# Kernel optimization log

Hardware: AMD Instinct MI355X
Metric: run time of the kernel (lower is better)

## Reference

```python
import jax, jax.numpy as jnp
import numpy as np

B, N, NODE_DIM, COND_DIM, EDGE_DIM = 32, 96, 2048, 1024, 128


def _wn_linear(x, v, g, b):
    # weight-normed linear: W = g * v / ||v||_row  (torch nn.utils.weight_norm, dim=0)
    w = v * (g / jnp.linalg.norm(v, axis=1))[:, None]
    return x @ w.T + b


def setup_inputs() -> dict:
    key = jax.random.key(0)
    ks = jax.random.split(key, 6)

    def lin(k, out_d, in_d):
        k1, k2, k3 = jax.random.split(k, 3)
        v = jax.random.normal(k1, (out_d, in_d), jnp.float32) * (1.0 / np.sqrt(in_d))
        g = jax.random.uniform(k2, (out_d,), jnp.float32, 0.5, 1.5)
        b = jax.random.normal(k3, (out_d,), jnp.float32) * 0.01
        return v, g, b

    node_feats = jax.random.normal(ks[0], (B, N, NODE_DIM), jnp.float32)
    cond_feats = jax.random.normal(ks[1], (B, COND_DIM), jnp.float32)

    # edge indexes: flat indices into the [B*N*N] pairwise tensor, self-loops removed
    i, j = np.meshgrid(np.arange(N), np.arange(N), indexing='ij')
    pair = (i * N + j)[i != j]                                  # [N*(N-1)]
    edge_indexes = (np.arange(B)[:, None] * N * N + pair[None, :]).reshape(-1)
    edge_indexes = jnp.asarray(edge_indexes, dtype=jnp.int32)   # [B*N*(N-1)]

    node_v, node_g, node_b = lin(ks[2], EDGE_DIM, NODE_DIM)
    joint_v, joint_g, joint_b = lin(ks[3], EDGE_DIM, 2 * EDGE_DIM)
    q_v, q_g, q_b = lin(ks[4], EDGE_DIM, COND_DIM)
    lin_v, lin_g, lin_b = lin(ks[5], EDGE_DIM, 2 * EDGE_DIM)

    return {
        'node_feats': node_feats, 'cond_feats': cond_feats, 'edge_indexes': edge_indexes,
        'node_v': node_v, 'node_g': node_g, 'node_b': node_b,
        'joint_v': joint_v, 'joint_g': joint_g, 'joint_b': joint_b,
        'q_v': q_v, 'q_g': q_g, 'q_b': q_b,
        'lin_v': lin_v, 'lin_g': lin_g, 'lin_b': lin_b,
    }


def reference(node_feats, cond_feats, edge_indexes,
              node_v, node_g, node_b,
              joint_v, joint_g, joint_b,
              q_v, q_g, q_b,
              lin_v, lin_g, lin_b):
    b_n, n_n, _ = node_feats.shape
    # node projection (dropout p=0 -> identity)
    h = jax.nn.relu(_wn_linear(node_feats, node_v, node_g, node_b))   # [B, N, E]

    # node_intersect('cat') builds [B,N,N,2E] then flattens; we gather the
    # selected edges directly by decomposing the flat indices (same math).
    nn2 = n_n * n_n
    bi = edge_indexes // nn2
    rem = edge_indexes % nn2
    ii = rem // n_n
    jj = rem % n_n
    fusion = jnp.concatenate([h[bi, ii], h[bi, jj]], axis=-1)         # [Edges, 2E]

    joint = jax.nn.relu(_wn_linear(fusion, joint_v, joint_g, joint_b))  # [Edges, E]
    q = jax.nn.relu(_wn_linear(cond_feats, q_v, q_g, q_b))              # [B, E]

    e_per = joint.shape[0] // b_n
    o_c = joint.shape[1]
    jb = joint.reshape(b_n, e_per, o_c)
    qb = jnp.broadcast_to(q[:, None, :], (b_n, e_per, o_c))
    cat = jnp.concatenate([jb, qb], axis=-1)                           # [B, Eper, 2E]
    out = jax.nn.relu(_wn_linear(cat, lin_v, lin_g, lin_b))            # [B, Eper, E]
    return out.reshape(b_n * e_per, o_c)
```

## Files before the change

### kernel.cpp

```cpp
#include <hip/hip_runtime.h>
#include <hip/hip_bf16.h>


#define WS_BIAS      256
#define WS_WN_NODE   4096
#define WS_WN_JOINT  528384
#define WS_WN_Q      593920
#define WS_WN_LIN    856064
#define WS_H         921600
#define WS_P         1708032
#define WS_Q         3280896
#define WS_QC        4853760

typedef __bf16 bf16x8 __attribute__((ext_vector_type(8)));
typedef float  f32x4  __attribute__((ext_vector_type(4)));

union BF8 { bf16x8 v; ushort u[8]; uint4 q; };

__device__ __forceinline__ float b2f(ushort u){ union{uint i; float f;} c; c.i=(uint)u<<16; return c.f; }
__device__ __forceinline__ ushort f2b(float f){ union{float f; uint i;} c; c.f=f; uint i=c.i; return (ushort)((i + 0x7FFFu + ((i>>16)&1u))>>16); }
__device__ __forceinline__ float getv(const void* p, int i, int bf){
  return bf ? b2f(((const ushort*)p)[i]) : ((const float*)p)[i];
}

__device__ __forceinline__ int detect_bf(const void* g_node_g){
  const ushort* p = (const ushort*)g_node_g;
  float v = b2f(p[threadIdx.x & 63]);
  unsigned long long m = __ballot(v > 0.35f && v < 1.75f);
  return m == ~0ull;
}

__global__ __launch_bounds__(256) void k_norm(
    const void* v0,const void* g0,const void* b0,
    const void* v1,const void* g1,const void* b1,
    const void* v2,const void* g2,const void* b2_,
    const void* v3,const void* g3,const void* b3,
    const void* gq, char* ws){
  const int bf = detect_bf(gq);
  int m = blockIdx.x >> 7;
  int r = blockIdx.x & 127;
  const void* V; const void* G; const void* Bv; int C; ushort* dst;
  if      (m==0){ V=v0; G=g0; Bv=b0;  C=2048; dst=(ushort*)(ws+WS_WN_NODE); }
  else if (m==1){ V=v1; G=g1; Bv=b1;  C=256;  dst=(ushort*)(ws+WS_WN_JOINT); }
  else if (m==2){ V=v2; G=g2; Bv=b2_; C=1024; dst=(ushort*)(ws+WS_WN_Q); }
  else          { V=v3; G=g3; Bv=b3;  C=256;  dst=(ushort*)(ws+WS_WN_LIN); }
  int t = threadIdx.x;
  float xv[8];
  int nv = 0;
  float ss = 0.f;
  for (int c=t;c<C;c+=256){ float x = getv(V, r*C+c, bf); xv[nv++] = x; ss += x*x; }
  for (int d=32;d>0;d>>=1) ss += __shfl_down(ss, d, 64);
  __shared__ float part[4];
  if ((t&63)==0) part[t>>6] = ss;
  __syncthreads();
  float scale = getv(G, r, bf) * rsqrtf(part[0]+part[1]+part[2]+part[3]);
  nv = 0;
  for (int c=t;c<C;c+=256) dst[r*C+c] = f2b(xv[nv++]*scale);
  if (r==0 && t<128) ((float*)(ws + WS_BIAS + m*512))[t] = getv(Bv, t, bf);
}

__global__ __launch_bounds__(64) void k_h(const void* xg, const void* gq,
                                          const char* ws, ushort* h){
  const int bf = detect_bf(gq);
  const ushort* W = (const ushort*)(ws + WS_WN_NODE);
  const float* bias = (const float*)(ws + WS_BIAS + 0);
  int lane = threadIdx.x & 63;
  int gw = blockIdx.x;
  int mtile = gw >> 2, nq = gw & 3;
  int row = lane & 15, g = lane >> 4;
  size_t xr = (size_t)(mtile*16 + row);
  f32x4 acc[2] = {};
  #pragma unroll 4
  for (int kk=0; kk<64; kk++){
    int off = kk*32 + g*8;
    BF8 a;
    if (bf) {
      a.q = *(const uint4*)((const ushort*)xg + xr*2048 + off);
    } else {
      const float* xp = (const float*)xg + xr*2048 + off;
      float4 x0 = ((const float4*)xp)[0], x1 = ((const float4*)xp)[1];
      a.u[0]=f2b(x0.x); a.u[1]=f2b(x0.y); a.u[2]=f2b(x0.z); a.u[3]=f2b(x0.w);
      a.u[4]=f2b(x1.x); a.u[5]=f2b(x1.y); a.u[6]=f2b(x1.z); a.u[7]=f2b(x1.w);
    }
    #pragma unroll
    for (int nt=0; nt<2; nt++){
      int wr = (nq*2+nt)*16 + row;
      BF8 bv; bv.q = *(const uint4*)(W + (size_t)wr*2048 + off);
      acc[nt] = __builtin_amdgcn_mfma_f32_16x16x32_bf16(a.v, bv.v, acc[nt], 0,0,0);
    }
  }
  #pragma unroll
  for (int nt=0; nt<2; nt++){
    #pragma unroll
    for (int r2=0; r2<4; r2++){
      int hr = mtile*16 + g*4 + r2;
      int hc = (nq*2+nt)*16 + row;
      float v = acc[nt][r2] + bias[hc];
      h[(size_t)hr*128 + hc] = f2b(v>0.f? v:0.f);
    }
  }
}

__global__ __launch_bounds__(128) void k_pqqc(const void* cond, const void* gq,
                                              const char* ws, ushort* Pp, ushort* Qp,
                                              float* qc){
  const int bf = detect_bf(gq);
  if (blockIdx.x < 96){
    const ushort* h  = (const ushort*)(ws + WS_H);
    const ushort* Wj = (const ushort*)(ws + WS_WN_JOINT);
    const float* bj  = (const float*)(ws + WS_BIAS + 1*512);
    int wid = threadIdx.x >> 6, lane = threadIdx.x & 63;
    int mtile = blockIdx.x*2 + wid;
    int row = lane&15, g = lane>>4;
    float bjv[8];
    #pragma unroll
    for (int vt=0; vt<8; vt++) bjv[vt] = bj[vt*16 + row];
    f32x4 acc[16] = {};
    #pragma unroll
    for (int kk=0; kk<4; kk++){
      int off = kk*32 + g*8;
      BF8 a; a.q = *(const uint4*)(h + (size_t)(mtile*16+row)*128 + off);
      #pragma unroll
      for (int vt=0; vt<16; vt++){
        int wr = (vt&7)*16 + row;
        int woff = (vt>>3)*128 + off;
        BF8 bv; bv.q = *(const uint4*)(Wj + (size_t)wr*256 + woff);
        acc[vt] = __builtin_amdgcn_mfma_f32_16x16x32_bf16(a.v, bv.v, acc[vt], 0,0,0);
      }
    }
    #pragma unroll
    for (int vt=0; vt<16; vt++){
      ushort* dst = (vt<8)? Pp : Qp;
      float badd = (vt<8)? bjv[vt&7] : 0.f;
      #pragma unroll
      for (int r2=0;r2<4;r2++){
        int mr = mtile*16 + g*4 + r2;
        int col = (vt&7)*16 + row;
        dst[(size_t)mr*128 + col] = f2b(acc[vt][r2] + badd);
      }
    }
  } else {
    const ushort* Wq = (const ushort*)(ws + WS_WN_Q);
    const ushort* Wl = (const ushort*)(ws + WS_WN_LIN);
    const float* qb = (const float*)(ws + WS_BIAS + 2*512);
    const float* lb = (const float*)(ws + WS_BIAS + 3*512);
    __shared__ float cs[1024];
    __shared__ float qs[128];
    int b = blockIdx.x - 96, t = threadIdx.x;
    for (int ii=0; ii<8; ii++) cs[t*8+ii] = getv(cond, b*1024 + t*8+ii, bf);
    __syncthreads();
    float s = 0.f;
    for (int c8=0; c8<128; c8++){
      BF8 w; w.q = *(const uint4*)(Wq + (size_t)t*1024 + c8*8);
      #pragma unroll
      for (int ii=0;ii<8;ii++) s += b2f(w.u[ii]) * cs[c8*8+ii];
    }
    s += qb[t];
    qs[t] = s>0.f? s:0.f;
    __syncthreads();
    float s2 = 0.f;
    for (int c8=0; c8<16; c8++){
      BF8 w; w.q = *(const uint4*)(Wl + (size_t)t*256 + 128 + c8*8);
      #pragma unroll
      for (int ii=0;ii<8;ii++) s2 += b2f(w.u[ii]) * qs[c8*8+ii];
    }
    qc[b*128 + t] = s2 + lb[t];
  }
}

__global__ __launch_bounds__(512) void k_edge(const void* gq,
                                              const char* ws, void* out){
  const int bf = detect_bf(gq);
  const ushort* Pp = (const ushort*)(ws + WS_P);
  const ushort* Qp = (const ushort*)(ws + WS_Q);
  const float* qc = (const float*)(ws + WS_QC);
  const ushort* Wl = (const ushort*)(ws + WS_WN_LIN);
  __shared__ __align__(16) char wlds[32768 + 16384];
  float* qcl = (float*)(wlds + 32768);
  int t = threadIdx.x;
  #pragma unroll
  for (int it=0; it<4; it++){
    int cid = t + it*512;
    int r = cid >> 4, cb = cid & 15;
    uint4 src = *(const uint4*)(Wl + (size_t)r*256 + cb*8);
    *(uint4*)(wlds + r*256 + ((cb*16) ^ ((r&7)<<4))) = src;
  }
  {
    const float4* src = (const float4*)(qc) + t*2;
    float4* dst = (float4*)qcl + t*2;
    dst[0] = src[0]; dst[1] = src[1];
  }

  int wid = t>>6, lane = t&63;
  int row = lane&15, g = lane>>4;
  int wbase = blockIdx.x*256 + wid*32;

  int b2m[2]; const ushort* Pr[2]; const ushort* Qr[2];
  #pragma unroll
  for (int m=0;m<2;m++){
    int e = wbase + m*16 + row;
    int b = e / 9120;
    int k = e - b*9120;
    int i2 = k / 95;
    int r2 = k - i2*95;
    int j2 = r2 < i2 ? r2 : r2 + 1;
    b2m[m] = b;
    Pr[m] = Pp + (size_t)(b*96+i2)*128;
    Qr[m] = Qp + (size_t)(b*96+j2)*128;
  }
  __syncthreads();

  BF8 af[2][4];
  #pragma unroll
  for (int m=0;m<2;m++){
    BF8 pb[4], qb2[4];
    #pragma unroll
    for (int kk=0;kk<4;kk++){
      int off = kk*32 + g*8;
      pb[kk].q  = *(const uint4*)(Pr[m] + off);
      qb2[kk].q = *(const uint4*)(Qr[m] + off);
    }
    #pragma unroll
    for (int kk=0;kk<4;kk++){
      BF8 a;
      #pragma unroll
      for (int i=0;i<8;i++){
        float v = b2f(pb[kk].u[i]) + b2f(qb2[kk].u[i]);
        a.u[i] = f2b(v>0.f? v:0.f);
      }
      af[m][kk].q = a.q;
    }
  }

  f32x4 acc[2][8] = {};
  #pragma unroll
  for (int kk=0;kk<4;kk++){
    #pragma unroll
    for (int nt=0;nt<8;nt++){
      int wr = nt*16 + row;
      BF8 aw; aw.q = *(const uint4*)(wlds + wr*256 + ((kk*64 + g*16) ^ ((wr&7)<<4)));
      acc[0][nt] = __builtin_amdgcn_mfma_f32_16x16x32_bf16(aw.v, af[0][kk].v, acc[0][nt], 0,0,0);
      acc[1][nt] = __builtin_amdgcn_mfma_f32_16x16x32_bf16(aw.v, af[1][kk].v, acc[1][nt], 0,0,0);
    }
  }

  #pragma unroll
  for (int m=0;m<2;m++){
    const float* qcb = qcl + b2m[m]*128;
    size_t obase = (size_t)(wbase + m*16 + row)*128;
    #pragma unroll
    for (int nt=0;nt<8;nt++){
      int col0 = nt*16 + g*4;
      float4 q4 = *(const float4*)(qcb + col0);
      float v0 = acc[m][nt][0] + q4.x; v0 = v0>0.f? v0:0.f;
      float v1 = acc[m][nt][1] + q4.y; v1 = v1>0.f? v1:0.f;
      float v2 = acc[m][nt][2] + q4.z; v2 = v2>0.f? v2:0.f;
      float v3 = acc[m][nt][3] + q4.w; v3 = v3>0.f? v3:0.f;
      if (bf){
        union { ushort u[4]; ushort4 s; } o;
        o.u[0]=f2b(v0); o.u[1]=f2b(v1); o.u[2]=f2b(v2); o.u[3]=f2b(v3);
        *(ushort4*)((ushort*)out + obase + col0) = o.s;
      } else {
        float4 o; o.x=v0; o.y=v1; o.z=v2; o.w=v3;
        *(float4*)((float*)out + obase + col0) = o;
      }
    }
  }
}

extern "C" void kernel_launch(void* const* d_in, const int* in_sizes, int n_in,
                              void* d_out, int out_size, void* d_ws, size_t ws_size,
                              hipStream_t stream) {
  (void)in_sizes; (void)n_in; (void)out_size; (void)ws_size;
  char* ws = (char*)d_ws;
  const void* gq = d_in[4];
  k_norm<<<512, 256, 0, stream>>>(d_in[3], d_in[4], d_in[5],
                                  d_in[6], d_in[7], d_in[8],
                                  d_in[9], d_in[10], d_in[11],
                                  d_in[12], d_in[13], d_in[14], gq, ws);
  k_h<<<768, 64, 0, stream>>>(d_in[0], gq, ws, (ushort*)(ws + WS_H));
  k_pqqc<<<128, 128, 0, stream>>>(d_in[1], gq, ws,
                                  (ushort*)(ws + WS_P), (ushort*)(ws + WS_Q),
                                  (float*)(ws + WS_QC));
  k_edge<<<1140, 512, 0, stream>>>(gq, ws, d_out);
}
```

Before: 112.5 us.

## Fuse node projection with joint P/Q projection via LDS-resident h tile

Merges the node projection kernel and the P/Q/qc kernel into one launch. Each 256-thread block computes a 16-row tile of h, keeps it in shared memory, and immediately applies the joint weights, so h never goes to global memory. This removes one launch and the h round-trip. In exchange, only 224 blocks of 4 waves run the large node GEMM, compared with 768 single-wave blocks before, so there is less parallelism on the dominant stage.

```diff
diff --git a/kernel.cpp b/kernel.cpp
--- a/kernel.cpp
+++ b/kernel.cpp
@@ -7,7 +7,6 @@
 #define WS_WN_JOINT  528384
 #define WS_WN_Q      593920
 #define WS_WN_LIN    856064
-#define WS_H         921600
 #define WS_P         1708032
 #define WS_Q         3280896
 #define WS_QC        4853760
@@ -59,84 +58,76 @@
   if (r==0 && t<128) ((float*)(ws + WS_BIAS + m*512))[t] = getv(Bv, t, bf);
 }
 
-__global__ __launch_bounds__(64) void k_h(const void* xg, const void* gq,
-                                          const char* ws, ushort* h){
+__global__ __launch_bounds__(256) void k_hpq(const void* xg, const void* cond,
+                                             const void* gq, const char* ws,
+                                             ushort* Pp, ushort* Qp, float* qc){
   const int bf = detect_bf(gq);
-  const ushort* W = (const ushort*)(ws + WS_WN_NODE);
-  const float* bias = (const float*)(ws + WS_BIAS + 0);
-  int lane = threadIdx.x & 63;
-  int gw = blockIdx.x;
-  int mtile = gw >> 2, nq = gw & 3;
-  int row = lane & 15, g = lane >> 4;
-  size_t xr = (size_t)(mtile*16 + row);
-  f32x4 acc[2] = {};
-  #pragma unroll 4
-  for (int kk=0; kk<64; kk++){
-    int off = kk*32 + g*8;
-    BF8 a;
-    if (bf) {
-      a.q = *(const uint4*)((const ushort*)xg + xr*2048 + off);
-    } else {
-      const float* xp = (const float*)xg + xr*2048 + off;
-      float4 x0 = ((const float4*)xp)[0], x1 = ((const float4*)xp)[1];
-      a.u[0]=f2b(x0.x); a.u[1]=f2b(x0.y); a.u[2]=f2b(x0.z); a.u[3]=f2b(x0.w);
-      a.u[4]=f2b(x1.x); a.u[5]=f2b(x1.y); a.u[6]=f2b(x1.z); a.u[7]=f2b(x1.w);
-    }
-    #pragma unroll
-    for (int nt=0; nt<2; nt++){
-      int wr = (nq*2+nt)*16 + row;
-      BF8 bv; bv.q = *(const uint4*)(W + (size_t)wr*2048 + off);
-      acc[nt] = __builtin_amdgcn_mfma_f32_16x16x32_bf16(a.v, bv.v, acc[nt], 0,0,0);
-    }
-  }
-  #pragma unroll
-  for (int nt=0; nt<2; nt++){
-    #pragma unroll
-    for (int r2=0; r2<4; r2++){
-      int hr = mtile*16 + g*4 + r2;
-      int hc = (nq*2+nt)*16 + row;
-      float v = acc[nt][r2] + bias[hc];
-      h[(size_t)hr*128 + hc] = f2b(v>0.f? v:0.f);
-    }
-  }
-}
-
-__global__ __launch_bounds__(128) void k_pqqc(const void* cond, const void* gq,
-                                              const char* ws, ushort* Pp, ushort* Qp,
-                                              float* qc){
-  const int bf = detect_bf(gq);
-  if (blockIdx.x < 96){
-    const ushort* h  = (const ushort*)(ws + WS_H);
+  __shared__ __align__(16) ushort hl[2048];
+  __shared__ float cs[1024];
+  __shared__ float qs[128];
+  int t = threadIdx.x, wid = t>>6, lane = t&63;
+  int row = lane&15, g = lane>>4;
+  if (blockIdx.x < 192){
+    const ushort* W = (const ushort*)(ws + WS_WN_NODE);
+    const float* bias = (const float*)(ws + WS_BIAS + 0);
     const ushort* Wj = (const ushort*)(ws + WS_WN_JOINT);
     const float* bj  = (const float*)(ws + WS_BIAS + 1*512);
-    int wid = threadIdx.x >> 6, lane = threadIdx.x & 63;
-    int mtile = blockIdx.x*2 + wid;
-    int row = lane&15, g = lane>>4;
-    float bjv[8];
-    #pragma unroll
-    for (int vt=0; vt<8; vt++) bjv[vt] = bj[vt*16 + row];
-    f32x4 acc[16] = {};
+    int mtile = blockIdx.x, nq = wid;
+    size_t xr = (size_t)(mtile*16 + row);
+    f32x4 acc[2] = {};
+    #pragma unroll 4
+    for (int kk=0; kk<64; kk++){
+      int off = kk*32 + g*8;
+      BF8 a;
+      if (bf) {
+        a.q = *(const uint4*)((const ushort*)xg + xr*2048 + off);
+      } else {
+        const float* xp = (const float*)xg + xr*2048 + off;
+        float4 x0 = ((const float4*)xp)[0], x1 = ((const float4*)xp)[1];
+        a.u[0]=f2b(x0.x); a.u[1]=f2b(x0.y); a.u[2]=f2b(x0.z); a.u[3]=f2b(x0.w);
+        a.u[4]=f2b(x1.x); a.u[5]=f2b(x1.y); a.u[6]=f2b(x1.z); a.u[7]=f2b(x1.w);
+      }
+      #pragma unroll
+      for (int nt=0; nt<2; nt++){
+        int wr = (nq*2+nt)*16 + row;
+        BF8 bv; bv.q = *(const uint4*)(W + (size_t)wr*2048 + off);
+        acc[nt] = __builtin_amdgcn_mfma_f32_16x16x32_bf16(a.v, bv.v, acc[nt], 0,0,0);
+      }
+    }
+    #pragma unroll
+    for (int nt=0; nt<2; nt++){
+      #pragma unroll
+      for (int r2=0; r2<4; r2++){
+        int hr = g*4 + r2;
+        int hc = (nq*2+nt)*16 + row;
+        float v = acc[nt][r2] + bias[hc];
+        hl[((hc>>5)<<9) + ((hr + (((hc>>3)&3)<<4))<<3) + (hc&7)] = f2b(v>0.f? v:0.f);
+      }
+    }
+    __syncthreads();
+    f32x4 acc2[4] = {};
     #pragma unroll
     for (int kk=0; kk<4; kk++){
-      int off = kk*32 + g*8;
-      BF8 a; a.q = *(const uint4*)(h + (size_t)(mtile*16+row)*128 + off);
-      #pragma unroll
-      for (int vt=0; vt<16; vt++){
+      BF8 a; a.q = *(const uint4*)(hl + (kk<<9) + lane*8);
+      #pragma unroll
+      for (int v4=0; v4<4; v4++){
+        int vt = wid*4 + v4;
         int wr = (vt&7)*16 + row;
-        int woff = (vt>>3)*128 + off;
+        int woff = (vt>>3)*128 + kk*32 + g*8;
         BF8 bv; bv.q = *(const uint4*)(Wj + (size_t)wr*256 + woff);
-        acc[vt] = __builtin_amdgcn_mfma_f32_16x16x32_bf16(a.v, bv.v, acc[vt], 0,0,0);
-      }
-    }
-    #pragma unroll
-    for (int vt=0; vt<16; vt++){
+        acc2[v4] = __builtin_amdgcn_mfma_f32_16x16x32_bf16(a.v, bv.v, acc2[v4], 0,0,0);
+      }
+    }
+    #pragma unroll
+    for (int v4=0; v4<4; v4++){
+      int vt = wid*4 + v4;
       ushort* dst = (vt<8)? Pp : Qp;
-      float badd = (vt<8)? bjv[vt&7] : 0.f;
+      float badd = (vt<8)? bj[(vt&7)*16 + row] : 0.f;
       #pragma unroll
       for (int r2=0;r2<4;r2++){
         int mr = mtile*16 + g*4 + r2;
         int col = (vt&7)*16 + row;
-        dst[(size_t)mr*128 + col] = f2b(acc[vt][r2] + badd);
+        dst[(size_t)mr*128 + col] = f2b(acc2[v4][r2] + badd);
       }
     }
   } else {
@@ -144,27 +135,29 @@
     const ushort* Wl = (const ushort*)(ws + WS_WN_LIN);
     const float* qb = (const float*)(ws + WS_BIAS + 2*512);
     const float* lb = (const float*)(ws + WS_BIAS + 3*512);
-    __shared__ float cs[1024];
-    __shared__ float qs[128];
-    int b = blockIdx.x - 96, t = threadIdx.x;
-    for (int ii=0; ii<8; ii++) cs[t*8+ii] = getv(cond, b*1024 + t*8+ii, bf);
+    int b = blockIdx.x - 192;
+    for (int ii=0; ii<4; ii++) cs[t*4+ii] = getv(cond, b*1024 + t*4+ii, bf);
     __syncthreads();
-    float s = 0.f;
-    for (int c8=0; c8<128; c8++){
-      BF8 w; w.q = *(const uint4*)(Wq + (size_t)t*1024 + c8*8);
-      #pragma unroll
-      for (int ii=0;ii<8;ii++) s += b2f(w.u[ii]) * cs[c8*8+ii];
-    }
-    s += qb[t];
-    qs[t] = s>0.f? s:0.f;
+    if (t < 128){
+      float s = 0.f;
+      for (int c8=0; c8<128; c8++){
+        BF8 w; w.q = *(const uint4*)(Wq + (size_t)t*1024 + c8*8);
+        #pragma unroll
+        for (int ii=0;ii<8;ii++) s += b2f(w.u[ii]) * cs[c8*8+ii];
+      }
+      s += qb[t];
+      qs[t] = s>0.f? s:0.f;
+    }
     __syncthreads();
-    float s2 = 0.f;
-    for (int c8=0; c8<16; c8++){
-      BF8 w; w.q = *(const uint4*)(Wl + (size_t)t*256 + 128 + c8*8);
-      #pragma unroll
-      for (int ii=0;ii<8;ii++) s2 += b2f(w.u[ii]) * qs[c8*8+ii];
-    }
-    qc[b*128 + t] = s2 + lb[t];
+    if (t < 128){
+      float s2 = 0.f;
+      for (int c8=0; c8<16; c8++){
+        BF8 w; w.q = *(const uint4*)(Wl + (size_t)t*256 + 128 + c8*8);
+        #pragma unroll
+        for (int ii=0;ii<8;ii++) s2 += b2f(w.u[ii]) * qs[c8*8+ii];
+      }
+      qc[b*128 + t] = s2 + lb[t];
+    }
   }
 }
 
@@ -278,9 +271,8 @@
                                   d_in[6], d_in[7], d_in[8],
                                   d_in[9], d_in[10], d_in[11],
                                   d_in[12], d_in[13], d_in[14], gq, ws);
-  k_h<<<768, 64, 0, stream>>>(d_in[0], gq, ws, (ushort*)(ws + WS_H));
-  k_pqqc<<<128, 128, 0, stream>>>(d_in[1], gq, ws,
-                                  (ushort*)(ws + WS_P), (ushort*)(ws + WS_Q),
-                                  (float*)(ws + WS_QC));
+  k_hpq<<<224, 256, 0, stream>>>(d_in[0], d_in[1], gq, ws,
+                                 (ushort*)(ws + WS_P), (ushort*)(ws + WS_Q),
+                                 (float*)(ws + WS_QC));
   k_edge<<<1140, 512, 0, stream>>>(gq, ws, d_out);
 }
```

Result: faster. 92.89 us (median of 2 runs) (-17.4%).
